# Optimization experiments

Hardware: AMD Instinct MI355X
Metric: run time of the kernel (lower is better)

## Reference

```python
import jax, jax.numpy as jnp
import numpy as np
from math import sqrt

N_HEADS = 16

def _rope(t, freqs):
    # t: [b, n, l, hd]; freqs: [l, hd//2, 2] (real, imag of unit rotations)
    b, n, l, hd = t.shape
    t2 = t.reshape(b, n, l, hd // 2, 2)
    tr, ti = t2[..., 0], t2[..., 1]
    fr, fi = freqs[..., 0], freqs[..., 1]  # broadcast over b, n
    out_r = tr * fr - ti * fi
    out_i = tr * fi + ti * fr
    return jnp.stack([out_r, out_i], axis=-1).reshape(b, n, l, hd)

def setup_inputs() -> dict:
    key = jax.random.key(0)
    ks = jax.random.split(key, 6)
    B, L, D = 2, 2048, 1024
    HD = D // N_HEADS
    x = jax.random.normal(ks[0], (B, L, D), dtype=jnp.float32)
    # proper rotary frequencies: theta_i = 10000^{-2i/hd}, angle = pos * theta
    inv = 1.0 / (10000.0 ** (np.arange(0, HD, 2, dtype=np.float32) / HD))  # [HD//2]
    ang = np.arange(L, dtype=np.float32)[:, None] * inv[None, :]           # [L, HD//2]
    freqs = jnp.asarray(np.stack([np.cos(ang), np.sin(ang)], axis=-1))     # [L, HD//2, 2]
    # additive causal mask
    causal = jnp.tril(jnp.ones((L, L), dtype=bool))
    attention_mask = jnp.where(causal, 0.0, -1e9).astype(jnp.float32)[None, None]
    init = 1.0 / sqrt(D)
    Wq = jax.random.normal(ks[1], (D, D), dtype=jnp.float32) * init
    Wk = jax.random.normal(ks[2], (D, D), dtype=jnp.float32) * init
    Wv = jax.random.normal(ks[3], (D, D), dtype=jnp.float32) * init
    Wo = jax.random.normal(ks[4], (D, D), dtype=jnp.float32) * init
    return {"x": x, "freqs": freqs, "attention_mask": attention_mask,
            "Wq": Wq, "Wk": Wk, "Wv": Wv, "Wo": Wo}

def reference(x, freqs, attention_mask, Wq, Wk, Wv, Wo):
    b, l, d = x.shape
    n = N_HEADS
    hd = d // n
    scale = sqrt(hd)

    def split_heads(t):  # [b, l, d] -> [b, n, l, hd]
        return t.reshape(b, l, n, hd).transpose(0, 2, 1, 3)

    q = split_heads(x @ Wq.T)
    k = split_heads(x @ Wk.T)
    v = split_heads(x @ Wv.T)
    q = _rope(q, freqs)
    k = _rope(k, freqs)
    scores = jnp.einsum('bnqd,bnkd->bnqk', q, k) / scale
    attn = jax.nn.softmax(scores + attention_mask, axis=-1)
    out = jnp.einsum('bnqk,bnkd->bnqd', attn, v)
    out = out.transpose(0, 2, 1, 3).reshape(b, l, d)
    return out @ Wo.T
```

## Files before the change

kernel.cpp:

```cpp
#include <hip/hip_runtime.h>
#include <stdint.h>

#define LSEQ 2048
#define DMODEL 1024
#define NHEADS 16
#define HDIM 64
#define MROWS 4096

typedef __attribute__((ext_vector_type(8))) short short8;
typedef __attribute__((ext_vector_type(4))) float f32x4;
typedef __attribute__((ext_vector_type(16))) float f32x16;

static __device__ __forceinline__ unsigned short f2bf(float f) {
    unsigned u = __builtin_bit_cast(unsigned, f);
    u += 0x7fffu + ((u >> 16) & 1u);
    return (unsigned short)(u >> 16);
}
static __device__ __forceinline__ unsigned cvt_pk_bf16(float a, float b) {
    unsigned r;
    asm("v_cvt_pk_bf16_f32 %0, %1, %2" : "=v"(r) : "v"(a), "v"(b));
    return r;
}

static __device__ __forceinline__ void gl2lds16(const unsigned short* g, unsigned short* l) {
    __builtin_amdgcn_global_load_lds(
        (const __attribute__((address_space(1))) unsigned int*)g,
        (__attribute__((address_space(3))) unsigned int*)l, 16, 0, 0);
}

__global__ void cast_all(const float* __restrict__ x,  const float* __restrict__ Wq,
                         const float* __restrict__ Wk, const float* __restrict__ Wv,
                         const float* __restrict__ Wo,
                         unsigned short* __restrict__ xb,
                         unsigned short* __restrict__ wqkv,
                         unsigned short* __restrict__ wo) {
    int i = blockIdx.x * blockDim.x + threadIdx.x;
    const float4* src;
    ushort4* dst;
    if (i < 1048576) {
        src = (const float4*)x + i;
        dst = (ushort4*)xb + i;
    } else {
        int t = i - 1048576;
        int w = t >> 18;
        int j = t & 262143;
        const float* s = (w == 0) ? Wq : (w == 1) ? Wk : (w == 2) ? Wv : Wo;
        src = (const float4*)s + j;
        dst = (w == 3) ? ((ushort4*)wo + j) : ((ushort4*)wqkv + (size_t)w * 262144 + j);
    }
    float4 v = *src;
    ushort4 o;
    o.x = f2bf(v.x); o.y = f2bf(v.y); o.z = f2bf(v.z); o.w = f2bf(v.w);
    *dst = o;
}

template <int MODE, int NBY>
__global__ __launch_bounds__(256, 2) void gemm128(const unsigned short* __restrict__ A,
                                                  const unsigned short* __restrict__ Bw,
                                                  const float* __restrict__ freqs,
                                                  unsigned short* __restrict__ qh,
                                                  unsigned short* __restrict__ kh,
                                                  unsigned short* __restrict__ vt,
                                                  float* __restrict__ C) {
    extern __shared__ unsigned short lds[];

    int tid  = threadIdx.x;
    int lane = tid & 63, wave = tid >> 6;
    int row16 = lane & 15, quad = lane >> 4;
    int wm = wave & 1, wn = wave >> 1;

    int id  = blockIdx.x;
    int gid = (id & 7) * (4 * NBY) + (id >> 3);
    int bx = gid / NBY, by = gid % NBY;
    int m0 = bx * 128, n0 = by * 128;

    int off0 = tid * 16;
    int g = off0 ^ (((off0 >> 7) & 3) << 4);
    int srow = g >> 6;
    int scol = (g & 63) >> 1;
    const unsigned short* Ag = A  + (size_t)(m0 + srow) * DMODEL + scol;
    const unsigned short* Bg = Bw + (size_t)(n0 + srow) * DMODEL + scol;

    int sw   = ((row16 >> 1) & 3) << 4;
    int aoff = (wm * 64 + row16) * 32 + (((quad * 16) ^ sw) >> 1);
    int boff = (wn * 64 + row16) * 32 + (((quad * 16) ^ sw) >> 1);

    f32x4 acc[4][4];
    #pragma unroll
    for (int i = 0; i < 4; ++i)
        #pragma unroll
        for (int j = 0; j < 4; ++j) acc[i][j] = (f32x4){0.f, 0.f, 0.f, 0.f};

    auto stage = [&](int t) {
        int bo = (t & 1) * 16384;
        const unsigned short* As_ = Ag + t * 64;
        const unsigned short* Bs_ = Bg + t * 64;
        gl2lds16(As_,                 lds + bo + 0     + wave * 512);
        gl2lds16(As_ + 64 * DMODEL,   lds + bo + 2048  + wave * 512);
        gl2lds16(As_ + 32,            lds + bo + 4096  + wave * 512);
        gl2lds16(As_ + 32 + 64 * DMODEL, lds + bo + 6144 + wave * 512);
        gl2lds16(Bs_,                 lds + bo + 8192  + wave * 512);
        gl2lds16(Bs_ + 64 * DMODEL,   lds + bo + 10240 + wave * 512);
        gl2lds16(Bs_ + 32,            lds + bo + 12288 + wave * 512);
        gl2lds16(Bs_ + 32 + 64 * DMODEL, lds + bo + 14336 + wave * 512);
    };

    stage(0);
    stage(1);

    for (int t = 0; t < 16; ++t) {
        if (t < 15) asm volatile("s_waitcnt vmcnt(8)" ::: "memory");
        else        asm volatile("s_waitcnt vmcnt(0)" ::: "memory");
        __builtin_amdgcn_s_barrier();
        __builtin_amdgcn_sched_barrier(0);

        int bo = (t & 1) * 16384;
        #pragma unroll
        for (int kk = 0; kk < 2; ++kk) {
            short8 af[4], bfr[4];
            const unsigned short* Ap = lds + bo + kk * 4096 + aoff;
            const unsigned short* Bp = lds + bo + 8192 + kk * 4096 + boff;
            #pragma unroll
            for (int i = 0; i < 4; ++i) af[i] = *(const short8*)(Ap + i * 512);
            #pragma unroll
            for (int j = 0; j < 4; ++j) bfr[j] = *(const short8*)(Bp + j * 512);
            __builtin_amdgcn_s_setprio(1);
            #pragma unroll
            for (int i = 0; i < 4; ++i)
                #pragma unroll
                for (int j = 0; j < 4; ++j)
                    acc[i][j] = __builtin_amdgcn_mfma_f32_16x16x32_bf16(af[i], bfr[j], acc[i][j], 0, 0, 0);
            __builtin_amdgcn_s_setprio(0);
        }

        __builtin_amdgcn_sched_barrier(0);
        __builtin_amdgcn_s_barrier();
        if (t + 2 < 16) stage(t + 2);
    }

    int orow0 = m0 + wm * 64 + quad * 4;
    int ocol0 = n0 + wn * 64 + row16;

    if (MODE == 1) {
        #pragma unroll
        for (int mi = 0; mi < 4; ++mi)
            #pragma unroll
            for (int ni = 0; ni < 4; ++ni)
                #pragma unroll
                for (int r = 0; r < 4; ++r)
                    C[(size_t)(orow0 + mi * 16 + r) * DMODEL + (ocol0 + ni * 16)] = acc[mi][ni][r];
        return;
    }

    int region = n0 >> 10;
    int b = m0 >> 11;

    if (region < 2) {
        unsigned short* dst = region ? kh : qh;
        float sgn = (row16 & 1) ? 1.f : -1.f;
        #pragma unroll
        for (int nf = 0; nf < 4; ++nf) {
            int c = ocol0 - region * 1024 + nf * 16;
            int head = c >> 6, d = c & 63, ii = d >> 1;
            unsigned short* hb = dst + ((size_t)(b * NHEADS + head) * LSEQ) * HDIM + d;
            #pragma unroll
            for (int mf = 0; mf < 4; ++mf)
                #pragma unroll
                for (int r = 0; r < 4; ++r) {
                    int l = (orow0 + mf * 16 + r) & 2047;
                    float own = acc[mf][nf][r];
                    float par = __shfl_xor(own, 1);
                    float2 f = *(const float2*)(freqs + ((size_t)l * 32 + ii) * 2);
                    float out = own * f.x + par * (sgn * f.y);
                    hb[(size_t)l * HDIM] = f2bf(out);
                }
        }
    } else {
        #pragma unroll
        for (int nf = 0; nf < 4; ++nf) {
            int c = ocol0 - 2048 + nf * 16;
            int head = c >> 6, d = c & 63;
            size_t vbase = ((size_t)(b * NHEADS + head) * HDIM + d) * LSEQ;
            #pragma unroll
            for (int mf = 0; mf < 4; ++mf) {
                int l0 = (orow0 + mf * 16) & 2047;
                ushort4 o;
                o.x = f2bf(acc[mf][nf][0]);
                o.y = f2bf(acc[mf][nf][1]);
                o.z = f2bf(acc[mf][nf][2]);
                o.w = f2bf(acc[mf][nf][3]);
                *(ushort4*)(vt + vbase + l0) = o;
            }
        }
    }
}

__global__ __launch_bounds__(256, 4) void attn_flash(const unsigned short* __restrict__ qh,
                                                     const unsigned short* __restrict__ kh,
                                                     const unsigned short* __restrict__ vt,
                                                     unsigned short* __restrict__ oh) {
    __shared__ char smem[33280];
    unsigned short* ldsb = (unsigned short*)smem;
    float* mO = (float*)smem;
    float* mL = (float*)(smem + 16384);
    const float CS = 0.18033688011112042f;
    const float CB = 28.853900817779268f;

    int lane = threadIdx.x & 63;
    int wave = threadIdx.x >> 6;
    int l31 = lane & 31;
    int h   = lane >> 5;
    int kq  = wave >> 1, qq = wave & 1;

    int id  = blockIdx.x;
    int xcd = id & 7;
    int bn  = xcd * 4 + ((id >> 3) & 3);
    int p   = id >> 5;
    int b = bn >> 4, n = bn & 15;

    const unsigned short* Qb = qh + (size_t)bn * LSEQ * HDIM;
    const unsigned short* Kb = kh + (size_t)bn * LSEQ * HDIM;
    const unsigned short* Vb = vt + (size_t)bn * HDIM * LSEQ;

    int sf  = wave >> 1;
    int m0s = (wave & 1) * 2;
    const unsigned short* kg = Kb + (size_t)(sf * 32 + l31) * HDIM + m0s * 16 + h * 8;
    const unsigned short* vg = Vb + (size_t)(sf * 32 + l31) * LSEQ + m0s * 16 + h * 8;
    int soff = (sf * 4 + m0s) * 512;

    auto stage = [&](int t) {
        int sl = (t & 1) * 4096;
        const unsigned short* kgk = kg + (size_t)t * 64 * HDIM;
        const unsigned short* vgk = vg + t * 64;
        gl2lds16(kgk,      ldsb + sl + soff);
        gl2lds16(kgk + 16, ldsb + sl + soff + 512);
        gl2lds16(vgk,      ldsb + 8192 + sl + soff);
        gl2lds16(vgk + 16, ldsb + 8192 + sl + soff + 512);
    };

    auto run_qb = [&](int qb) {
        int q0 = qb * 64;
        int qabs = q0 + qq * 32 + l31;

        short8 qf[4];
        #pragma unroll
        for (int mf = 0; mf < 4; ++mf)
            qf[mf] = *(const short8*)(Qb + (size_t)(q0 + qq * 32 + l31) * HDIM + mf * 16 + h * 8);

        f32x16 accO[2];
        #pragma unroll
        for (int i = 0; i < 16; ++i) { accO[0][i] = 0.f; accO[1][i] = 0.f; }
        float l_s = 0.f;

        int nk = qb + 1;

        stage(0);
        stage(1);

        for (int kt = 0; kt < nk; ++kt) {
            if (kt < nk - 1) asm volatile("s_waitcnt vmcnt(4)" ::: "memory");
            else             asm volatile("s_waitcnt vmcnt(0)" ::: "memory");
            __builtin_amdgcn_s_barrier();
            __builtin_amdgcn_sched_barrier(0);

            int cb = (kt & 1) * 4096;
            const unsigned short* Kc = ldsb + cb;
            const unsigned short* Vc = ldsb + 8192 + cb;

            bool edge = (kt == nk - 1);
            bool dead = edge && (kq == 1) && (qq == 0);

            if (!dead) {
                f32x16 z;
                #pragma unroll
                for (int i = 0; i < 16; ++i) z[i] = 0.f;
                __builtin_amdgcn_s_setprio(1);
                #pragma unroll
                for (int m = 0; m < 4; ++m) {
                    short8 kf = *(const short8*)(Kc + (kq * 4 + m) * 512 + lane * 8);
                    z = __builtin_amdgcn_mfma_f32_32x32x16_bf16(kf, qf[m], z, 0, 0, 0);
                }
                __builtin_amdgcn_s_setprio(0);

                float p_[16];
                bool maskz = edge && (kq == qq);
                #pragma unroll
                for (int r = 0; r < 16; ++r) {
                    float e = __builtin_amdgcn_exp2f(z[r] * CS - CB);
                    if (maskz) {
                        int kabs = kt * 64 + kq * 32 + (r & 3) + 8 * (r >> 2) + 4 * h;
                        if (kabs > qabs) e = 0.f;
                    }
                    p_[r] = e;
                }
                float ps = 0.f;
                #pragma unroll
                for (int r = 0; r < 16; ++r) ps += p_[r];
                l_s += ps;

                uint2 P4[4];
                #pragma unroll
                for (int g = 0; g < 4; ++g) {
                    P4[g].x = cvt_pk_bf16(p_[4 * g],     p_[4 * g + 1]);
                    P4[g].y = cvt_pk_bf16(p_[4 * g + 2], p_[4 * g + 3]);
                }
                short8 bfr[2];
                bool hb = (h != 0);
                #pragma unroll
                for (int m = 0; m < 2; ++m) {
                    uint2 own = hb ? P4[1 + 2 * m] : P4[2 * m];
                    uint2 snd = hb ? P4[2 * m]     : P4[1 + 2 * m];
                    uint2 rcv;
                    rcv.x = __shfl_xor(snd.x, 32);
                    rcv.y = __shfl_xor(snd.y, 32);
                    uint4 bb;
                    bb.x = hb ? rcv.x : own.x;
                    bb.y = hb ? rcv.y : own.y;
                    bb.z = hb ? own.x : rcv.x;
                    bb.w = hb ? own.y : rcv.y;
                    bfr[m] = __builtin_bit_cast(short8, bb);
                }

                __builtin_amdgcn_s_setprio(1);
                #pragma unroll
                for (int dq = 0; dq < 2; ++dq)
                    #pragma unroll
                    for (int m = 0; m < 2; ++m) {
                        short8 vf = *(const short8*)(Vc + (dq * 4 + kq * 2 + m) * 512 + lane * 8);
                        accO[dq] = __builtin_amdgcn_mfma_f32_32x32x16_bf16(vf, bfr[m], accO[dq], 0, 0, 0);
                    }
                __builtin_amdgcn_s_setprio(0);
            }

            __builtin_amdgcn_sched_barrier(0);
            __builtin_amdgcn_s_barrier();
            if (kt + 2 < nk) stage(kt + 2);
        }

        l_s += __shfl_xor(l_s, 32);

        if (kq == 1) {
            #pragma unroll
            for (int dq = 0; dq < 2; ++dq)
                #pragma unroll
                for (int r = 0; r < 16; ++r)
                    mO[(qq * 2 + dq) * 1024 + r * 64 + lane] = accO[dq][r];
            mL[qq * 64 + lane] = l_s;
        }
        __syncthreads();
        if (kq == 0) {
            float inv = 1.0f / (l_s + mL[qq * 64 + lane]);
            #pragma unroll
            for (int dq = 0; dq < 2; ++dq)
                #pragma unroll
                for (int g = 0; g < 4; ++g) {
                    float o0 = (accO[dq][4 * g]     + mO[(qq * 2 + dq) * 1024 + (4 * g)     * 64 + lane]) * inv;
                    float o1 = (accO[dq][4 * g + 1] + mO[(qq * 2 + dq) * 1024 + (4 * g + 1) * 64 + lane]) * inv;
                    float o2 = (accO[dq][4 * g + 2] + mO[(qq * 2 + dq) * 1024 + (4 * g + 2) * 64 + lane]) * inv;
                    float o3 = (accO[dq][4 * g + 3] + mO[(qq * 2 + dq) * 1024 + (4 * g + 3) * 64 + lane]) * inv;
                    ushort4 o;
                    o.x = f2bf(o0); o.y = f2bf(o1); o.z = f2bf(o2); o.w = f2bf(o3);
                    int d = dq * 32 + 8 * g + 4 * h;
                    *(ushort4*)(oh + (size_t)(b * LSEQ + q0 + qq * 32 + l31) * DMODEL + n * HDIM + d) = o;
                }
        }
        __syncthreads();
    };

    run_qb(31 - p);
    run_qb(p);
}

extern "C" void kernel_launch(void* const* d_in, const int* in_sizes, int n_in,
                              void* d_out, int out_size, void* d_ws, size_t ws_size,
                              hipStream_t stream) {
    const float* x     = (const float*)d_in[0];
    const float* freqs = (const float*)d_in[1];
    const float* Wq = (const float*)d_in[3];
    const float* Wk = (const float*)d_in[4];
    const float* Wv = (const float*)d_in[5];
    const float* Wo = (const float*)d_in[6];

    char* ws = (char*)d_ws;
    unsigned short* xb   = (unsigned short*)ws; ws += (size_t)MROWS * DMODEL * 2;
    unsigned short* wqkv = (unsigned short*)ws; ws += (size_t)3 * DMODEL * DMODEL * 2;
    unsigned short* wo   = (unsigned short*)ws; ws += (size_t)DMODEL * DMODEL * 2;
    unsigned short* qh   = (unsigned short*)ws; ws += (size_t)32 * LSEQ * HDIM * 2;
    unsigned short* kh   = (unsigned short*)ws; ws += (size_t)32 * LSEQ * HDIM * 2;
    unsigned short* vt   = (unsigned short*)ws; ws += (size_t)32 * HDIM * LSEQ * 2;
    unsigned short* oh   = (unsigned short*)ws; ws += (size_t)MROWS * DMODEL * 2;

    static bool attr_set = false;
    if (!attr_set) {
        (void)hipFuncSetAttribute((const void*)gemm128<0, 24>,
                                  hipFuncAttributeMaxDynamicSharedMemorySize, 65536);
        (void)hipFuncSetAttribute((const void*)gemm128<1, 8>,
                                  hipFuncAttributeMaxDynamicSharedMemorySize, 65536);
        attr_set = true;
    }

    cast_all<<<8192, 256, 0, stream>>>(x, Wq, Wk, Wv, Wo, xb, wqkv, wo);

    gemm128<0, 24><<<768, 256, 65536, stream>>>(xb, wqkv, freqs, qh, kh, vt, nullptr);

    attn_flash<<<512, 256, 0, stream>>>(qh, kh, vt, oh);

    gemm128<1, 8><<<256, 256, 65536, stream>>>(oh, wo, nullptr, nullptr, nullptr, nullptr, (float*)d_out);
}
```

Measured before the change: 186.1 us.

## Process paired query blocks in one KV sweep to share K/V tile loads

Each block already handled two query blocks (31-p and p) one after the other, streaming K/V twice. The new flash loop walks the K/V tiles once for the longer block and also computes the shorter block while the tiles are resident, sharing K fragments from LDS and V fragments across both accumulators. It also drops the occupancy hint from launch bounds, which allows more registers for the doubled accumulators, and reverses the p mapping for alternating blocks to spread work. The costs are higher register pressure, possibly lower occupancy, and a doB branch inside the inner loop.

```diff
diff --git a/kernel.cpp b/kernel.cpp
--- a/kernel.cpp
+++ b/kernel.cpp
@@ -195,10 +195,10 @@
     }
 }
 
-__global__ __launch_bounds__(256, 4) void attn_flash(const unsigned short* __restrict__ qh,
-                                                     const unsigned short* __restrict__ kh,
-                                                     const unsigned short* __restrict__ vt,
-                                                     unsigned short* __restrict__ oh) {
+__global__ __launch_bounds__(256) void attn_flash(const unsigned short* __restrict__ qh,
+                                                  const unsigned short* __restrict__ kh,
+                                                  const unsigned short* __restrict__ vt,
+                                                  unsigned short* __restrict__ oh) {
     __shared__ char smem[33280];
     unsigned short* ldsb = (unsigned short*)smem;
     float* mO = (float*)smem;
@@ -215,12 +215,25 @@
     int id  = blockIdx.x;
     int xcd = id & 7;
     int bn  = xcd * 4 + ((id >> 3) & 3);
-    int p   = id >> 5;
+    int praw = id >> 5;
+    int p = ((id >> 3) & 1) ? (15 - praw) : praw;
     int b = bn >> 4, n = bn & 15;
 
     const unsigned short* Qb = qh + (size_t)bn * LSEQ * HDIM;
     const unsigned short* Kb = kh + (size_t)bn * LSEQ * HDIM;
     const unsigned short* Vb = vt + (size_t)bn * HDIM * LSEQ;
+
+    int qbA = 31 - p, qbB = p;
+    int q0A = qbA * 64, q0B = qbB * 64;
+    int qabsA = q0A + qq * 32 + l31;
+    int qabsB = q0B + qq * 32 + l31;
+
+    short8 qfA[4], qfB[4];
+    #pragma unroll
+    for (int mf = 0; mf < 4; ++mf) {
+        qfA[mf] = *(const short8*)(Qb + (size_t)(q0A + qq * 32 + l31) * HDIM + mf * 16 + h * 8);
+        qfB[mf] = *(const short8*)(Qb + (size_t)(q0B + qq * 32 + l31) * HDIM + mf * 16 + h * 8);
+    }
 
     int sf  = wave >> 1;
     int m0s = (wave & 1) * 2;
@@ -238,73 +251,79 @@
         gl2lds16(vgk + 16, ldsb + 8192 + sl + soff + 512);
     };
 
-    auto run_qb = [&](int qb) {
-        int q0 = qb * 64;
-        int qabs = q0 + qq * 32 + l31;
-
-        short8 qf[4];
-        #pragma unroll
-        for (int mf = 0; mf < 4; ++mf)
-            qf[mf] = *(const short8*)(Qb + (size_t)(q0 + qq * 32 + l31) * HDIM + mf * 16 + h * 8);
-
-        f32x16 accO[2];
-        #pragma unroll
-        for (int i = 0; i < 16; ++i) { accO[0][i] = 0.f; accO[1][i] = 0.f; }
-        float l_s = 0.f;
-
-        int nk = qb + 1;
-
-        stage(0);
-        stage(1);
-
-        for (int kt = 0; kt < nk; ++kt) {
-            if (kt < nk - 1) asm volatile("s_waitcnt vmcnt(4)" ::: "memory");
-            else             asm volatile("s_waitcnt vmcnt(0)" ::: "memory");
-            __builtin_amdgcn_s_barrier();
-            __builtin_amdgcn_sched_barrier(0);
-
-            int cb = (kt & 1) * 4096;
-            const unsigned short* Kc = ldsb + cb;
-            const unsigned short* Vc = ldsb + 8192 + cb;
-
-            bool edge = (kt == nk - 1);
-            bool dead = edge && (kq == 1) && (qq == 0);
-
-            if (!dead) {
-                f32x16 z;
-                #pragma unroll
-                for (int i = 0; i < 16; ++i) z[i] = 0.f;
+    f32x16 accA[2], accB[2];
+    #pragma unroll
+    for (int i = 0; i < 16; ++i) { accA[0][i] = 0.f; accA[1][i] = 0.f; accB[0][i] = 0.f; accB[1][i] = 0.f; }
+    float lA = 0.f, lB = 0.f;
+
+    int nk = qbA + 1;
+
+    stage(0);
+    stage(1);
+
+    for (int kt = 0; kt < nk; ++kt) {
+        if (kt < nk - 1) asm volatile("s_waitcnt vmcnt(4)" ::: "memory");
+        else             asm volatile("s_waitcnt vmcnt(0)" ::: "memory");
+        __builtin_amdgcn_s_barrier();
+        __builtin_amdgcn_sched_barrier(0);
+
+        int cb = (kt & 1) * 4096;
+        const unsigned short* Kc = ldsb + cb;
+        const unsigned short* Vc = ldsb + 8192 + cb;
+
+        bool edgeA = (kt == qbA);
+        bool deadA = edgeA && (kq == 1) && (qq == 0);
+        bool doB   = (kt <= qbB) && !((kt == qbB) && (kq == 1) && (qq == 0));
+
+        if (!deadA) {
+            short8 kf[4];
+            #pragma unroll
+            for (int m = 0; m < 4; ++m)
+                kf[m] = *(const short8*)(Kc + (kq * 4 + m) * 512 + lane * 8);
+
+            f32x16 zA;
+            #pragma unroll
+            for (int i = 0; i < 16; ++i) zA[i] = 0.f;
+            __builtin_amdgcn_s_setprio(1);
+            #pragma unroll
+            for (int m = 0; m < 4; ++m)
+                zA = __builtin_amdgcn_mfma_f32_32x32x16_bf16(kf[m], qfA[m], zA, 0, 0, 0);
+            __builtin_amdgcn_s_setprio(0);
+
+            f32x16 zB;
+            if (doB) {
+                #pragma unroll
+                for (int i = 0; i < 16; ++i) zB[i] = 0.f;
                 __builtin_amdgcn_s_setprio(1);
                 #pragma unroll
-                for (int m = 0; m < 4; ++m) {
-                    short8 kf = *(const short8*)(Kc + (kq * 4 + m) * 512 + lane * 8);
-                    z = __builtin_amdgcn_mfma_f32_32x32x16_bf16(kf, qf[m], z, 0, 0, 0);
-                }
+                for (int m = 0; m < 4; ++m)
+                    zB = __builtin_amdgcn_mfma_f32_32x32x16_bf16(kf[m], qfB[m], zB, 0, 0, 0);
                 __builtin_amdgcn_s_setprio(0);
-
+            }
+
+            short8 bfrA[2];
+            {
                 float p_[16];
-                bool maskz = edge && (kq == qq);
+                bool mz = edgeA && (kq == qq);
                 #pragma unroll
                 for (int r = 0; r < 16; ++r) {
-                    float e = __builtin_amdgcn_exp2f(z[r] * CS - CB);
-                    if (maskz) {
+                    float e = __builtin_amdgcn_exp2f(zA[r] * CS - CB);
+                    if (mz) {
                         int kabs = kt * 64 + kq * 32 + (r & 3) + 8 * (r >> 2) + 4 * h;
-                        if (kabs > qabs) e = 0.f;
+                        if (kabs > qabsA) e = 0.f;
                     }
                     p_[r] = e;
                 }
                 float ps = 0.f;
                 #pragma unroll
                 for (int r = 0; r < 16; ++r) ps += p_[r];
-                l_s += ps;
-
+                lA += ps;
                 uint2 P4[4];
                 #pragma unroll
-                for (int g = 0; g < 4; ++g) {
-                    P4[g].x = cvt_pk_bf16(p_[4 * g],     p_[4 * g + 1]);
-                    P4[g].y = cvt_pk_bf16(p_[4 * g + 2], p_[4 * g + 3]);
-                }
-                short8 bfr[2];
+                for (int g2 = 0; g2 < 4; ++g2) {
+                    P4[g2].x = cvt_pk_bf16(p_[4 * g2],     p_[4 * g2 + 1]);
+                    P4[g2].y = cvt_pk_bf16(p_[4 * g2 + 2], p_[4 * g2 + 3]);
+                }
                 bool hb = (h != 0);
                 #pragma unroll
                 for (int m = 0; m < 2; ++m) {
@@ -318,27 +337,70 @@
                     bb.y = hb ? rcv.y : own.y;
                     bb.z = hb ? own.x : rcv.x;
                     bb.w = hb ? own.y : rcv.y;
-                    bfr[m] = __builtin_bit_cast(short8, bb);
-                }
-
-                __builtin_amdgcn_s_setprio(1);
-                #pragma unroll
-                for (int dq = 0; dq < 2; ++dq)
-                    #pragma unroll
-                    for (int m = 0; m < 2; ++m) {
-                        short8 vf = *(const short8*)(Vc + (dq * 4 + kq * 2 + m) * 512 + lane * 8);
-                        accO[dq] = __builtin_amdgcn_mfma_f32_32x32x16_bf16(vf, bfr[m], accO[dq], 0, 0, 0);
+                    bfrA[m] = __builtin_bit_cast(short8, bb);
+                }
+            }
+
+            short8 bfrB[2];
+            if (doB) {
+                float p_[16];
+                bool mz = (kt == qbB) && (kq == qq);
+                #pragma unroll
+                for (int r = 0; r < 16; ++r) {
+                    float e = __builtin_amdgcn_exp2f(zB[r] * CS - CB);
+                    if (mz) {
+                        int kabs = kt * 64 + kq * 32 + (r & 3) + 8 * (r >> 2) + 4 * h;
+                        if (kabs > qabsB) e = 0.f;
                     }
-                __builtin_amdgcn_s_setprio(0);
+                    p_[r] = e;
+                }
+                float ps = 0.f;
+                #pragma unroll
+                for (int r = 0; r < 16; ++r) ps += p_[r];
+                lB += ps;
+                uint2 P4[4];
+                #pragma unroll
+                for (int g2 = 0; g2 < 4; ++g2) {
+                    P4[g2].x = cvt_pk_bf16(p_[4 * g2],     p_[4 * g2 + 1]);
+                    P4[g2].y = cvt_pk_bf16(p_[4 * g2 + 2], p_[4 * g2 + 3]);
+                }
+                bool hb = (h != 0);
+                #pragma unroll
+                for (int m = 0; m < 2; ++m) {
+                    uint2 own = hb ? P4[1 + 2 * m] : P4[2 * m];
+                    uint2 snd = hb ? P4[2 * m]     : P4[1 + 2 * m];
+                    uint2 rcv;
+                    rcv.x = __shfl_xor(snd.x, 32);
+                    rcv.y = __shfl_xor(snd.y, 32);
+                    uint4 bb;
+                    bb.x = hb ? rcv.x : own.x;
+                    bb.y = hb ? rcv.y : own.y;
+                    bb.z = hb ? own.x : rcv.x;
+                    bb.w = hb ? own.y : rcv.y;
+                    bfrB[m] = __builtin_bit_cast(short8, bb);
+                }
             }
 
-            __builtin_amdgcn_sched_barrier(0);
-            __builtin_amdgcn_s_barrier();
-            if (kt + 2 < nk) stage(kt + 2);
-        }
-
+            __builtin_amdgcn_s_setprio(1);
+            #pragma unroll
+            for (int dq = 0; dq < 2; ++dq)
+                #pragma unroll
+                for (int m = 0; m < 2; ++m) {
+                    short8 vf = *(const short8*)(Vc + (dq * 4 + kq * 2 + m) * 512 + lane * 8);
+                    accA[dq] = __builtin_amdgcn_mfma_f32_32x32x16_bf16(vf, bfrA[m], accA[dq], 0, 0, 0);
+                    if (doB)
+                        accB[dq] = __builtin_amdgcn_mfma_f32_32x32x16_bf16(vf, bfrB[m], accB[dq], 0, 0, 0);
+                }
+            __builtin_amdgcn_s_setprio(0);
+        }
+
+        __builtin_amdgcn_sched_barrier(0);
+        __builtin_amdgcn_s_barrier();
+        if (kt + 2 < nk) stage(kt + 2);
+    }
+
+    auto epi = [&](int q0, f32x16* accO, float l_s) {
         l_s += __shfl_xor(l_s, 32);
-
         if (kq == 1) {
             #pragma unroll
             for (int dq = 0; dq < 2; ++dq)
@@ -353,22 +415,22 @@
             #pragma unroll
             for (int dq = 0; dq < 2; ++dq)
                 #pragma unroll
-                for (int g = 0; g < 4; ++g) {
-                    float o0 = (accO[dq][4 * g]     + mO[(qq * 2 + dq) * 1024 + (4 * g)     * 64 + lane]) * inv;
-                    float o1 = (accO[dq][4 * g + 1] + mO[(qq * 2 + dq) * 1024 + (4 * g + 1) * 64 + lane]) * inv;
-                    float o2 = (accO[dq][4 * g + 2] + mO[(qq * 2 + dq) * 1024 + (4 * g + 2) * 64 + lane]) * inv;
-                    float o3 = (accO[dq][4 * g + 3] + mO[(qq * 2 + dq) * 1024 + (4 * g + 3) * 64 + lane]) * inv;
+                for (int g2 = 0; g2 < 4; ++g2) {
+                    float o0 = (accO[dq][4 * g2]     + mO[(qq * 2 + dq) * 1024 + (4 * g2)     * 64 + lane]) * inv;
+                    float o1 = (accO[dq][4 * g2 + 1] + mO[(qq * 2 + dq) * 1024 + (4 * g2 + 1) * 64 + lane]) * inv;
+                    float o2 = (accO[dq][4 * g2 + 2] + mO[(qq * 2 + dq) * 1024 + (4 * g2 + 2) * 64 + lane]) * inv;
+                    float o3 = (accO[dq][4 * g2 + 3] + mO[(qq * 2 + dq) * 1024 + (4 * g2 + 3) * 64 + lane]) * inv;
                     ushort4 o;
                     o.x = f2bf(o0); o.y = f2bf(o1); o.z = f2bf(o2); o.w = f2bf(o3);
-                    int d = dq * 32 + 8 * g + 4 * h;
+                    int d = dq * 32 + 8 * g2 + 4 * h;
                     *(ushort4*)(oh + (size_t)(b * LSEQ + q0 + qq * 32 + l31) * DMODEL + n * HDIM + d) = o;
                 }
         }
         __syncthreads();
     };
 
-    run_qb(31 - p);
-    run_qb(p);
+    epi(q0A, accA, lA);
+    epi(q0B, accB, lB);
 }
 
 extern "C" void kernel_launch(void* const* d_in, const int* in_sizes, int n_in,
```

After: 186.6 us. About the same (+0.3%).
